# Optimization experiments

Measured on AMD Instinct MI355X. Metric: run time of the kernel, lower is better.

## Reference

```python
import jax, jax.numpy as jnp
import numpy as np

DIM = 384
HEADS = 12
WIN = (2, 7, 7)
MLP_RATIO = 4.0
EPS = 1e-5


def _rel_index(Wt, Wh, Ww):
    t, h, w = np.meshgrid(np.arange(Wt), np.arange(Wh), np.arange(Ww), indexing='ij')
    coords = np.stack([t, h, w]).reshape(3, -1).T  # (N,3)
    rel = coords[:, None] - coords[None]  # (N,N,3)
    rel[..., 0] += Wt - 1
    rel[..., 1] += Wh - 1
    rel[..., 2] += Ww - 1
    rel[..., 0] *= (2 * Wh - 1) * (2 * Ww - 1)
    rel[..., 1] *= (2 * Ww - 1)
    return rel.sum(-1)  # (N,N) int


def setup_inputs() -> dict:
    key = jax.random.key(0)
    ks = jax.random.split(key, 16)
    d = DIM
    hdim = int(d * MLP_RATIO)
    Wt, Wh, Ww = WIN
    table_size = (2 * Wt - 1) * (2 * Wh - 1) * (2 * Ww - 1)
    s = lambda fan: 1.0 / np.sqrt(fan)
    return {
        'x': jax.random.normal(ks[0], (2, 8, 56, 56, d), jnp.float32),
        'norm1_g': jnp.ones((d,), jnp.float32),
        'norm1_b': jnp.zeros((d,), jnp.float32),
        'qkv_w': jax.random.normal(ks[1], (d, 3 * d), jnp.float32) * s(d),
        'qkv_b': jnp.zeros((3 * d,), jnp.float32),
        'proj_w': jax.random.normal(ks[2], (d, d), jnp.float32) * s(d),
        'proj_b': jnp.zeros((d,), jnp.float32),
        'bias_table': jax.random.normal(ks[3], (table_size, HEADS), jnp.float32) * 0.02,
        'norm2_g': jnp.ones((d,), jnp.float32),
        'norm2_b': jnp.zeros((d,), jnp.float32),
        'fc1_w': jax.random.normal(ks[4], (d, hdim), jnp.float32) * s(d),
        'fc1_b': jnp.zeros((hdim,), jnp.float32),
        'fc2_w': jax.random.normal(ks[5], (hdim, d), jnp.float32) * s(hdim),
        'fc2_b': jnp.zeros((d,), jnp.float32),
        'rel_index': jnp.asarray(_rel_index(*WIN), jnp.int32),
    }


def _ln(x, g, b):
    mu = x.mean(-1, keepdims=True)
    var = ((x - mu) ** 2).mean(-1, keepdims=True)
    return (x - mu) * jax.lax.rsqrt(var + EPS) * g + b


def _window_partition(x, win):
    B, T, H, W, C = x.shape
    Wt, Wh, Ww = win
    x = x.reshape(B, T // Wt, Wt, H // Wh, Wh, W // Ww, Ww, C)
    x = x.transpose(0, 1, 3, 5, 2, 4, 6, 7)
    return x.reshape(-1, Wt * Wh * Ww, C)


def _window_reverse(win_x, win, B, T, H, W):
    Wt, Wh, Ww = win
    C = win_x.shape[-1]
    x = win_x.reshape(B, T // Wt, H // Wh, W // Ww, Wt, Wh, Ww, C)
    x = x.transpose(0, 1, 4, 2, 5, 3, 6, 7)
    return x.reshape(B, T, H, W, C)


def reference(x, norm1_g, norm1_b, qkv_w, qkv_b, proj_w, proj_b, bias_table,
              norm2_g, norm2_b, fc1_w, fc1_b, fc2_w, fc2_b, rel_index):
    B, T, H, W, C = x.shape
    Wt, Wh, Ww = WIN
    N = Wt * Wh * Ww
    shift = (Wt // 2, Wh // 2, Ww // 2)
    head_dim = C // HEADS
    scale = head_dim ** -0.5

    shortcut = x
    h = _ln(x, norm1_g, norm1_b)
    h = jnp.roll(h, shift=(-shift[0], -shift[1], -shift[2]), axis=(1, 2, 3))
    # dims chosen divisible by window -> no padding branch
    wins = _window_partition(h, WIN)  # (BnW, N, C)
    BnW = wins.shape[0]

    qkv = wins @ qkv_w + qkv_b  # (BnW, N, 3C)
    qkv = qkv.reshape(BnW, N, 3, HEADS, head_dim).transpose(2, 0, 3, 1, 4)
    q, k, v = qkv[0] * scale, qkv[1], qkv[2]  # (BnW, H, N, d)

    bias = bias_table[rel_index.reshape(-1)].reshape(N, N, HEADS).transpose(2, 0, 1)
    attn = jnp.einsum('bhnd,bhmd->bhnm', q, k) + bias[None]
    attn = jax.nn.softmax(attn, axis=-1)
    out = jnp.einsum('bhnm,bhmd->bhnd', attn, v)
    out = out.transpose(0, 2, 1, 3).reshape(BnW, N, C)
    out = out @ proj_w + proj_b

    h = _window_reverse(out.reshape(-1, Wt, Wh, Ww, C), WIN, B, T, H, W)
    h = jnp.roll(h, shift=shift, axis=(1, 2, 3))
    x = shortcut + h

    h2 = _ln(x, norm2_g, norm2_b)
    h2 = jax.nn.gelu(h2 @ fc1_w + fc1_b, approximate=False) @ fc2_w + fc2_b
    return x + h2
```

## Files before the change

### kernel.cpp

```cpp
#include <hip/hip_runtime.h>
#include <cstdint>
#include <cstddef>


typedef __bf16 bf16x8 __attribute__((ext_vector_type(8)));
typedef __bf16 bf16x4 __attribute__((ext_vector_type(4)));
typedef float f32x4 __attribute__((ext_vector_type(4)));

#define DIM 384
#define QKV_DIM 1152
#define HID 1536
#define NHEADS 12
#define NTOK 50176
#define NWIN 512

__device__ __forceinline__ void gload16(const void* g, void* s) {
  __builtin_amdgcn_global_load_lds(
      (const __attribute__((address_space(1))) void*)g,
      (__attribute__((address_space(3))) void*)s, 16, 0, 0);
}

__global__ __launch_bounds__(256) void build_tokmap_k(int* __restrict__ map) {
  int t = blockIdx.x * 256 + threadIdx.x;
  if (t >= NTOK) return;
  int win = t / 98, n = t - win * 98;
  int b = win >> 8, tw = (win >> 6) & 3, hw = (win >> 3) & 7, ww = win & 7;
  int dt = n / 49; int rem = n - dt * 49; int dh = rem / 7, dw = rem - dh * 7;
  int t0 = (tw * 2 + dt + 1) & 7;
  int h0 = hw * 7 + dh + 3; if (h0 >= 56) h0 -= 56;
  int w0 = ww * 7 + dw + 3; if (w0 >= 56) w0 -= 56;
  map[t] = ((b * 8 + t0) * 56 + h0) * 56 + w0;
}

__global__ __launch_bounds__(256) void expand_biasp_k(const float* __restrict__ table,
                                                      const int* __restrict__ rel,
                                                      float* __restrict__ out) {
  int e = blockIdx.x * 256 + threadIdx.x;
  if (e >= NHEADS * 49 * 256) return;
  int r = e & 3, l = (e >> 2) & 63;
  int rest = e >> 8;
  int ni = rest % 7, mi = (rest / 7) % 7, h = rest / 49;
  int i = mi * 16 + (l >> 4) * 4 + r;
  int j = ni * 16 + (l & 15);
  float v;
  if (j >= 98) v = -1e30f;
  else if (i >= 98) v = 0.f;
  else v = table[rel[i * 98 + j] * NHEADS + h];
  out[e] = v;
}

__global__ __launch_bounds__(256) void pack_w_k(const float* __restrict__ W,
                                                __bf16* __restrict__ WP,
                                                int K, int N, int nk,
                                                int scaleCols, float scale) {
  int idx = blockIdx.x * 256 + threadIdx.x;
  if (idx >= (K * N) >> 3) return;
  int l = idx & 63, f = (idx >> 6) & 7;
  int rest = idx >> 9, kt = rest % nk, cn = rest / nk;
  int n = f >> 1, kk = f & 1;
  int col = cn * 64 + n * 16 + (l & 15);
  int k0 = kt * 64 + (kk * 4 + (l >> 4)) * 8;
  float sc = (col < scaleCols) ? scale : 1.0f;
  bf16x8 v;
  #pragma unroll
  for (int j = 0; j < 8; ++j)
    v[j] = (__bf16)(W[(size_t)(k0 + j) * N + col] * sc);
  *(bf16x8*)(WP + (size_t)idx * 8) = v;
}

__global__ __launch_bounds__(256) void scale_bias_k(const float* __restrict__ b,
                                                    float* __restrict__ out,
                                                    int n, int scaleCols, float scale) {
  int e = blockIdx.x * 256 + threadIdx.x;
  if (e >= n) return;
  out[e] = b[e] * (e < scaleCols ? scale : 1.0f);
}

__global__ __launch_bounds__(384) void vtrans_k(const __bf16* __restrict__ qkv,
                                                __bf16* __restrict__ vt) {
  int win = blockIdx.x, t = threadIdx.x;
  const __bf16* base = qkv + (size_t)win * 98 * QKV_DIM + 768 + t;
  __bf16* orow = vt + ((size_t)win * 384 + t) * 128;
  #pragma unroll
  for (int c = 0; c < 16; ++c) {
    bf16x8 pk;
    #pragma unroll
    for (int e2 = 0; e2 < 8; ++e2) {
      int tok = c * 8 + e2;
      pk[e2] = (tok < 98) ? base[(size_t)tok * QKV_DIM] : (__bf16)0.f;
    }
    *(bf16x8*)(orow + c * 8) = pk;
  }
}

template <typename T>
__global__ __launch_bounds__(256) void ln_k(const T* __restrict__ x,
                                            const float* __restrict__ g,
                                            const float* __restrict__ bta,
                                            __bf16* __restrict__ out,
                                            const int* __restrict__ map) {
  int w = threadIdx.x >> 6, l = threadIdx.x & 63;
  int tok = blockIdx.x * 4 + w;
  int src = map ? map[tok] : tok;
  const T* row = x + (size_t)src * DIM;
  float v[6]; float s = 0.f;
  #pragma unroll
  for (int j = 0; j < 6; ++j) { v[j] = (float)row[l + 64 * j]; s += v[j]; }
  #pragma unroll
  for (int m = 1; m < 64; m <<= 1) s += __shfl_xor(s, m, 64);
  float mu = s * (1.f / DIM);
  float var = 0.f;
  #pragma unroll
  for (int j = 0; j < 6; ++j) { float d = v[j] - mu; var += d * d; }
  #pragma unroll
  for (int m = 1; m < 64; m <<= 1) var += __shfl_xor(var, m, 64);
  float rs = rsqrtf(var * (1.f / DIM) + 1e-5f);
  __bf16* orow = out + (size_t)tok * DIM;
  #pragma unroll
  for (int j = 0; j < 6; ++j) {
    int c = l + 64 * j;
    orow[c] = (__bf16)((v[j] - mu) * rs * g[c] + bta[c]);
  }
}

template <int EPI>
__global__ __launch_bounds__(256) void gemm_k(const __bf16* __restrict__ A,
                                              const __bf16* __restrict__ WP,
                                              const float* __restrict__ bias,
                                              int M, int N, int K,
                                              __bf16* __restrict__ outb,
                                              float* __restrict__ outf,
                                              const float* __restrict__ residf,
                                              const __bf16* __restrict__ residb,
                                              const int* __restrict__ tokmap) {
  __shared__ __align__(1024) char lds[32768];
  const int tid = threadIdx.x;
  const int l = tid & 63, w = tid >> 6;
  const int lr = l & 15, lg = l >> 4;
  const int ntile = N >> 6;
  const int nwg = gridDim.x, qd = nwg >> 3, rm = nwg & 7;
  const int xcd = blockIdx.x & 7;
  const int wgid = (xcd < rm ? xcd * (qd + 1) : rm * (qd + 1) + (xcd - rm) * qd)
                   + (blockIdx.x >> 3);
  const int bm = wgid / ntile, bn = wgid - bm * ntile;
  const int m0 = (bm << 8) + (w << 6);
  const int n0 = bn << 6;
  const int nk = K >> 6;
  const int sch = (l & 7) ^ ((l >> 3) & 7);
  const __bf16* pa = A + (size_t)(m0 + (l >> 3)) * K + sch * 8;
  char* abuf = lds + (w << 13);
  const __bf16* pB = WP + (size_t)bn * nk * 4096 + l * 8;

#define STAGEA(kt)                                                   \
  {                                                                  \
    const size_t ko_ = (size_t)(kt) << 6;                            \
    _Pragma("unroll")                                                \
    for (int s_ = 0; s_ < 8; ++s_)                                   \
      gload16(pa + (size_t)(s_ * 8) * K + ko_, abuf + s_ * 1024);    \
  }
#define LOADB(kt)                                                    \
  {                                                                  \
    const __bf16* p_ = pB + (size_t)(kt) * 4096;                     \
    _Pragma("unroll")                                                \
    for (int f_ = 0; f_ < 8; ++f_)                                   \
      b[f_] = *(const bf16x8*)(p_ + f_ * 512);                       \
  }
#define LDA()                                                        \
  {                                                                  \
    _Pragma("unroll")                                                \
    for (int kk_ = 0; kk_ < 2; ++kk_) {                              \
      const int ck_ = (kk_ << 2) + lg;                               \
      _Pragma("unroll")                                              \
      for (int m_ = 0; m_ < 4; ++m_) {                               \
        int r_ = (m_ << 4) + lr;                                     \
        a[m_][kk_] = *(const bf16x8*)(abuf + (r_ << 7) +             \
                                      ((ck_ ^ (r_ & 7)) << 4));      \
      }                                                              \
    }                                                                \
    asm volatile("s_waitcnt lgkmcnt(0)" ::: "memory");               \
    __builtin_amdgcn_sched_barrier(0);                               \
  }

  bf16x8 a[4][2], b[8];
  f32x4 acc[4][4] = {};

  STAGEA(0)
  asm volatile("s_waitcnt vmcnt(0)" ::: "memory");
  LDA()

  for (int kt = 0; kt < nk; ++kt) {
    LOADB(kt)
    const bool pf = (kt + 1 < nk);
    if (pf) STAGEA(kt + 1)
    __builtin_amdgcn_s_setprio(1);
    #pragma unroll
    for (int kk = 0; kk < 2; ++kk)
      #pragma unroll
      for (int m = 0; m < 4; ++m)
        #pragma unroll
        for (int n = 0; n < 4; ++n)
          acc[m][n] = __builtin_amdgcn_mfma_f32_16x16x32_bf16(b[n * 2 + kk], a[m][kk],
                                                              acc[m][n], 0, 0, 0);
    __builtin_amdgcn_s_setprio(0);
    if (pf) {
      asm volatile("s_waitcnt vmcnt(0)" ::: "memory");
      LDA()
    }
  }
#undef STAGEA
#undef LOADB
#undef LDA

  #pragma unroll
  for (int m = 0; m < 4; ++m) {
    const int grow = m0 + (m << 4) + lr;
    #pragma unroll
    for (int n = 0; n < 4; ++n) {
      const int gcol = n0 + (n << 4) + (lg << 2);
      f32x4 a4 = acc[m][n] + *(const f32x4*)(bias + gcol);
      if (EPI == 0) {
        bf16x4 c;
        #pragma unroll
        for (int r = 0; r < 4; ++r) c[r] = (__bf16)a4[r];
        *(bf16x4*)(outb + (size_t)grow * N + gcol) = c;
      } else if (EPI == 1) {
        int dst = tokmap[grow];
        f32x4 rv = *(const f32x4*)(residf + (size_t)dst * DIM + gcol);
        bf16x4 c;
        #pragma unroll
        for (int r = 0; r < 4; ++r) c[r] = (__bf16)(rv[r] + a4[r]);
        *(bf16x4*)(outb + (size_t)dst * DIM + gcol) = c;
      } else if (EPI == 2) {
        bf16x4 c;
        #pragma unroll
        for (int r = 0; r < 4; ++r) {
          float vv = a4[r];
          float y = vv * (1.0f + 0.044715f * vv * vv);
          c[r] = (__bf16)(vv / (1.0f + __expf(-1.5957691216057308f * y)));
        }
        *(bf16x4*)(outb + (size_t)grow * N + gcol) = c;
      } else {
        bf16x4 sv = *(const bf16x4*)(residb + (size_t)grow * N + gcol);
        f32x4 o;
        #pragma unroll
        for (int r = 0; r < 4; ++r) o[r] = (float)sv[r] + a4[r];
        *(f32x4*)(outf + (size_t)grow * N + gcol) = o;
      }
    }
  }
}

__global__ __launch_bounds__(64) void attn_k(const __bf16* __restrict__ qkv,
                                             const __bf16* __restrict__ vt,
                                             const float* __restrict__ pb,
                                             __bf16* __restrict__ out) {
  __shared__ __align__(1024) char P[4096];
  const int l = threadIdx.x, lr = l & 15, lg = l >> 4;
  const int bid = blockIdx.x;
  const int xc = bid & 7, kk = bid >> 3;
  const int wh = (kk / 7) * 8 + xc, mi = kk % 7;
  const int win = wh / NHEADS, h = wh - win * NHEADS;
  const size_t wbase = (size_t)win * 98 * QKV_DIM;
  const __bf16* qb = qkv + wbase + h * 32;
  const __bf16* kb = qb + 384;
  const bf16x8 z8 = {};
  const f32x4 fz = {};

  bf16x8 kf[7];
  #pragma unroll
  for (int ni = 0; ni < 7; ++ni) {
    int tok = ni * 16 + lr;
    kf[ni] = (tok < 98) ? *(const bf16x8*)(kb + (size_t)tok * QKV_DIM + lg * 8) : z8;
  }
  int qt = mi * 16 + lr;
  bf16x8 qf = (qt < 98) ? *(const bf16x8*)(qb + (size_t)qt * QKV_DIM + lg * 8) : z8;
  const f32x4* pbp = (const f32x4*)pb + (size_t)((h * 7 + mi) * 7) * 64 + l;
  f32x4 bv[7];
  #pragma unroll
  for (int ni = 0; ni < 7; ++ni) bv[ni] = pbp[ni * 64];

  f32x4 s[7];
  #pragma unroll
  for (int ni = 0; ni < 7; ++ni)
    s[ni] = __builtin_amdgcn_mfma_f32_16x16x32_bf16(qf, kf[ni], fz, 0, 0, 0);

  if (l < 32) {
    int row = l >> 1, c = 14 + (l & 1);
    *(f32x4*)(P + row * 256 + ((c ^ (row & 7)) << 4)) = fz;
  }

  #pragma unroll
  for (int r = 0; r < 4; ++r) {
    float mx = -1e30f;
    #pragma unroll
    for (int ni = 0; ni < 7; ++ni) {
      float vv = s[ni][r] + bv[ni][r];
      s[ni][r] = vv;
      mx = fmaxf(mx, vv);
    }
    #pragma unroll
    for (int m2 = 1; m2 < 16; m2 <<= 1) mx = fmaxf(mx, __shfl_xor(mx, m2, 64));
    float sum = 0.f;
    #pragma unroll
    for (int ni = 0; ni < 7; ++ni) { float p = __expf(s[ni][r] - mx); s[ni][r] = p; sum += p; }
    #pragma unroll
    for (int m2 = 1; m2 < 16; m2 <<= 1) sum += __shfl_xor(sum, m2, 64);
    float inv = 1.0f / sum;
    int il = lg * 4 + r;
    #pragma unroll
    for (int ni = 0; ni < 7; ++ni) {
      int j = ni * 16 + lr;
      *(__bf16*)(P + il * 256 + (((j >> 3) ^ (il & 7)) << 4) + ((j & 7) << 1)) =
          (__bf16)(s[ni][r] * inv);
    }
  }
  __syncthreads();

  bf16x8 pa[4];
  #pragma unroll
  for (int ks = 0; ks < 4; ++ks) {
    int ck = ks * 4 + lg;
    pa[ks] = *(const bf16x8*)(P + lr * 256 + ((ck ^ (lr & 7)) << 4));
  }
  const __bf16* vrow = vt + ((size_t)wh * 32) * 128;
  __bf16* ob = out + ((size_t)win * 98 + mi * 16) * DIM + h * 32;
  #pragma unroll
  for (int nf = 0; nf < 2; ++nf) {
    int d = nf * 16 + lr;
    f32x4 o = fz;
    #pragma unroll
    for (int ks = 0; ks < 4; ++ks) {
      bf16x8 vb = *(const bf16x8*)(vrow + (size_t)d * 128 + ks * 32 + lg * 8);
      o = __builtin_amdgcn_mfma_f32_16x16x32_bf16(pa[ks], vb, o, 0, 0, 0);
    }
    #pragma unroll
    for (int r = 0; r < 4; ++r) {
      int il = lg * 4 + r;
      if (mi * 16 + il < 98) ob[(size_t)il * DIM + nf * 16 + lr] = (__bf16)o[r];
    }
  }
}

extern "C" void kernel_launch(void* const* d_in, const int* in_sizes, int n_in,
                              void* d_out, int out_size, void* d_ws, size_t ws_size,
                              hipStream_t stream) {
  const float* x      = (const float*)d_in[0];
  const float* n1g    = (const float*)d_in[1];
  const float* n1b    = (const float*)d_in[2];
  const float* qkv_w  = (const float*)d_in[3];
  const float* qkv_b  = (const float*)d_in[4];
  const float* proj_w = (const float*)d_in[5];
  const float* proj_b = (const float*)d_in[6];
  const float* btab   = (const float*)d_in[7];
  const float* n2g    = (const float*)d_in[8];
  const float* n2b    = (const float*)d_in[9];
  const float* fc1_w  = (const float*)d_in[10];
  const float* fc1_b  = (const float*)d_in[11];
  const float* fc2_w  = (const float*)d_in[12];
  const float* fc2_b  = (const float*)d_in[13];
  const int*   relidx = (const int*)d_in[14];
  float* outp = (float*)d_out;
  (void)in_sizes; (void)n_in; (void)out_size; (void)ws_size;

  char* ws = (char*)d_ws;
  size_t off = 0;
  auto alloc = [&](size_t bytes) {
    char* p = ws + off;
    off = (off + bytes + 255) & ~(size_t)255;
    return p;
  };
  int*    tokmap = (int*)alloc((size_t)NTOK * 4);
  float*  biasex = (float*)alloc((size_t)NHEADS * 49 * 256 * 4);
  __bf16* wqkvP  = (__bf16*)alloc((size_t)QKV_DIM * DIM * 2);
  __bf16* wprojP = (__bf16*)alloc((size_t)DIM * DIM * 2);
  __bf16* wfc1P  = (__bf16*)alloc((size_t)HID * DIM * 2);
  __bf16* wfc2P  = (__bf16*)alloc((size_t)DIM * HID * 2);
  float*  qkvbS  = (float*)alloc((size_t)QKV_DIM * 4);
  __bf16* tokens = (__bf16*)alloc((size_t)NTOK * DIM * 2);
  __bf16* qkvbuf = (__bf16*)alloc((size_t)NTOK * HID * 2);
  __bf16* s1     = (__bf16*)alloc((size_t)NTOK * DIM * 2);
  __bf16* attnout = tokens;
  __bf16* h1 = qkvbuf;
  __bf16* vt = (__bf16*)d_out;

  const float scale = 0.17677669529663687f;

  build_tokmap_k<<<NTOK / 256, 256, 0, stream>>>(tokmap);
  expand_biasp_k<<<(NHEADS * 49 * 256) / 256, 256, 0, stream>>>(btab, relidx, biasex);
  pack_w_k<<<(DIM * QKV_DIM / 8) / 256, 256, 0, stream>>>(qkv_w, wqkvP, DIM, QKV_DIM, 6, DIM, scale);
  pack_w_k<<<(DIM * DIM / 8) / 256, 256, 0, stream>>>(proj_w, wprojP, DIM, DIM, 6, 0, 1.0f);
  pack_w_k<<<(DIM * HID / 8) / 256, 256, 0, stream>>>(fc1_w, wfc1P, DIM, HID, 6, 0, 1.0f);
  pack_w_k<<<(HID * DIM / 8) / 256, 256, 0, stream>>>(fc2_w, wfc2P, HID, DIM, 24, 0, 1.0f);
  scale_bias_k<<<(QKV_DIM + 255) / 256, 256, 0, stream>>>(qkv_b, qkvbS, QKV_DIM, DIM, scale);

  ln_k<float><<<NTOK / 4, 256, 0, stream>>>(x, n1g, n1b, tokens, tokmap);
  gemm_k<0><<<(NTOK / 256) * (QKV_DIM / 64), 256, 0, stream>>>(
      tokens, wqkvP, qkvbS, NTOK, QKV_DIM, DIM, qkvbuf, nullptr, nullptr, nullptr, nullptr);
  vtrans_k<<<NWIN, 384, 0, stream>>>(qkvbuf, vt);
  attn_k<<<NWIN * NHEADS * 7, 64, 0, stream>>>(qkvbuf, vt, biasex, attnout);
  gemm_k<1><<<(NTOK / 256) * (DIM / 64), 256, 0, stream>>>(
      attnout, wprojP, proj_b, NTOK, DIM, DIM, s1, nullptr, x, nullptr, tokmap);
  ln_k<__bf16><<<NTOK / 4, 256, 0, stream>>>(s1, n2g, n2b, tokens, nullptr);
  gemm_k<2><<<(NTOK / 256) * (HID / 64), 256, 0, stream>>>(
      tokens, wfc1P, fc1_b, NTOK, HID, DIM, h1, nullptr, nullptr, nullptr, nullptr);
  gemm_k<3><<<(NTOK / 256) * (DIM / 64), 256, 0, stream>>>(
      h1, wfc2P, fc2_b, NTOK, DIM, HID, nullptr, outp, nullptr, s1, nullptr);
}
```

Measured before the change: 520.7 us.

## Add A-stationary deep GEMM for K=384 layers and coalesce transposes via LDS

Adds a GEMM kernel for the K=384 layers (qkv, proj, fc1) in which each workgroup loads a 64-row A block once into LDS and loops over 128-column output groups. Weight fragments are double-buffered in registers, and the weights are repacked into a 128-wide layout to match. This removes the repeated A reloads of the old 256x64 tiling, at the cost of more LDS, more accumulators and less parallelism per workgroup. The V transpose and the attention output store now go through LDS, so global writes become full 16-byte rows instead of strided or scalar stores.

```diff
diff --git a/kernel.cpp b/kernel.cpp
--- a/kernel.cpp
+++ b/kernel.cpp
@@ -49,10 +49,28 @@
   out[e] = v;
 }
 
-__global__ __launch_bounds__(256) void pack_w_k(const float* __restrict__ W,
-                                                __bf16* __restrict__ WP,
-                                                int K, int N, int nk,
-                                                int scaleCols, float scale) {
+__global__ __launch_bounds__(256) void pack_w128_k(const float* __restrict__ W,
+                                                   __bf16* __restrict__ WP,
+                                                   int K, int N, int nk,
+                                                   int scaleCols, float scale) {
+  int idx = blockIdx.x * 256 + threadIdx.x;
+  if (idx >= (K * N) >> 3) return;
+  int l = idx & 63, f = (idx >> 6) & 7, wc = (idx >> 9) & 1;
+  int rest = idx >> 10, kt = rest % nk, bn = rest / nk;
+  int n = f >> 1, kk = f & 1;
+  int col = bn * 128 + wc * 64 + n * 16 + (l & 15);
+  int k0 = kt * 64 + (kk * 4 + (l >> 4)) * 8;
+  float sc = (col < scaleCols) ? scale : 1.0f;
+  bf16x8 v;
+  #pragma unroll
+  for (int j = 0; j < 8; ++j)
+    v[j] = (__bf16)(W[(size_t)(k0 + j) * N + col] * sc);
+  *(bf16x8*)(WP + (size_t)idx * 8) = v;
+}
+
+__global__ __launch_bounds__(256) void pack_w64_k(const float* __restrict__ W,
+                                                  __bf16* __restrict__ WP,
+                                                  int K, int N, int nk) {
   int idx = blockIdx.x * 256 + threadIdx.x;
   if (idx >= (K * N) >> 3) return;
   int l = idx & 63, f = (idx >> 6) & 7;
@@ -60,11 +78,10 @@
   int n = f >> 1, kk = f & 1;
   int col = cn * 64 + n * 16 + (l & 15);
   int k0 = kt * 64 + (kk * 4 + (l >> 4)) * 8;
-  float sc = (col < scaleCols) ? scale : 1.0f;
   bf16x8 v;
   #pragma unroll
   for (int j = 0; j < 8; ++j)
-    v[j] = (__bf16)(W[(size_t)(k0 + j) * N + col] * sc);
+    v[j] = (__bf16)W[(size_t)(k0 + j) * N + col];
   *(bf16x8*)(WP + (size_t)idx * 8) = v;
 }
 
@@ -78,9 +95,9 @@
 
 __global__ __launch_bounds__(384) void vtrans_k(const __bf16* __restrict__ qkv,
                                                 __bf16* __restrict__ vt) {
+  __shared__ __align__(1024) char T[98304];
   int win = blockIdx.x, t = threadIdx.x;
   const __bf16* base = qkv + (size_t)win * 98 * QKV_DIM + 768 + t;
-  __bf16* orow = vt + ((size_t)win * 384 + t) * 128;
   #pragma unroll
   for (int c = 0; c < 16; ++c) {
     bf16x8 pk;
@@ -89,7 +106,17 @@
       int tok = c * 8 + e2;
       pk[e2] = (tok < 98) ? base[(size_t)tok * QKV_DIM] : (__bf16)0.f;
     }
-    *(bf16x8*)(orow + c * 8) = pk;
+    *(bf16x8*)(T + t * 256 + ((c ^ (t & 15)) << 4)) = pk;
+  }
+  __syncthreads();
+  char* wb = (char*)(vt + (size_t)win * 49152);
+  #pragma unroll
+  for (int i = 0; i < 16; ++i) {
+    int g = i * 6144 + t * 16;
+    int row = g >> 8, p = (g >> 4) & 15;
+    bf16x8 v = *(const bf16x8*)(T + row * 256 + (p << 4));
+    int lc = p ^ (row & 15);
+    *(bf16x8*)(wb + row * 256 + (lc << 4)) = v;
   }
 }
 
@@ -124,16 +151,124 @@
 }
 
 template <int EPI>
-__global__ __launch_bounds__(256) void gemm_k(const __bf16* __restrict__ A,
-                                              const __bf16* __restrict__ WP,
-                                              const float* __restrict__ bias,
-                                              int M, int N, int K,
-                                              __bf16* __restrict__ outb,
-                                              float* __restrict__ outf,
-                                              const float* __restrict__ residf,
-                                              const __bf16* __restrict__ residb,
-                                              const int* __restrict__ tokmap) {
+__global__ __launch_bounds__(256) void gemm_deep_k(const __bf16* __restrict__ A,
+                                                   const __bf16* __restrict__ WP,
+                                                   const float* __restrict__ bias,
+                                                   int M, int N, int Gtot,
+                                                   __bf16* __restrict__ outb,
+                                                   const float* __restrict__ residf,
+                                                   const int* __restrict__ tokmap) {
+  __shared__ __align__(1024) char lds[49152];
+  const int K = 384;
+  const int tid = threadIdx.x;
+  const int l = tid & 63, w = tid >> 6;
+  const int lr = l & 15, lg = l >> 4;
+  const int bid = (blockIdx.x & 7) * (gridDim.x >> 3) + (blockIdx.x >> 3);
+  const int m0 = bid << 6;
+  const int sch = (l & 7) ^ ((l >> 3) & 7);
+  #pragma unroll
+  for (int i = 0; i < 12; ++i) {
+    const int c12 = w * 12 + i;
+    const int row = ((c12 & 7) << 3) + (l >> 3);
+    gload16(A + (size_t)(m0 + row) * K + ((c12 >> 3) << 6) + sch * 8,
+            lds + c12 * 1024);
+  }
+  __syncthreads();
+
+  const f32x4 fz4 = {};
+  f32x4 acc[4][8] = {};
+  bf16x8 b0[8], b1[8], af[4][2];
+
+#define LOADB(dst, p)                                          \
+  { _Pragma("unroll")                                          \
+    for (int f_ = 0; f_ < 8; ++f_)                             \
+      dst[f_] = *(const bf16x8*)((p) + f_ * 512); }
+#define LDA(kt)                                                \
+  { _Pragma("unroll")                                          \
+    for (int kk_ = 0; kk_ < 2; ++kk_) {                        \
+      const int ck_ = (kk_ << 2) + lg;                         \
+      _Pragma("unroll")                                        \
+      for (int m_ = 0; m_ < 4; ++m_) {                         \
+        const int r_ = (m_ << 4) + lr;                         \
+        af[m_][kk_] = *(const bf16x8*)(lds + (kt) * 8192 +     \
+            (r_ << 7) + ((ck_ ^ (r_ & 7)) << 4));              \
+      } }                                                      \
+    asm volatile("s_waitcnt lgkmcnt(0)" ::: "memory");         \
+    __builtin_amdgcn_sched_barrier(0); }
+#define MFMA_HALF(NOFF, B)                                     \
+  { __builtin_amdgcn_s_setprio(1);                             \
+    _Pragma("unroll")                                          \
+    for (int kk_ = 0; kk_ < 2; ++kk_)                          \
+      _Pragma("unroll")                                        \
+      for (int m_ = 0; m_ < 4; ++m_)                           \
+        _Pragma("unroll")                                      \
+        for (int n_ = 0; n_ < 4; ++n_)                         \
+          acc[m_][(NOFF) + n_] = __builtin_amdgcn_mfma_f32_16x16x32_bf16( \
+              B[n_ * 2 + kk_], af[m_][kk_], acc[m_][(NOFF) + n_], 0, 0, 0); \
+    __builtin_amdgcn_s_setprio(0); }
+
+  const __bf16* pg = WP + (size_t)w * 49152 + (size_t)l * 8;
+  if (w < Gtot) LOADB(b0, pg)
+  for (int g = w; g < Gtot; g += 4) {
+    #pragma unroll
+    for (int kt = 0; kt < 6; ++kt) {
+      const __bf16* ph = pg + kt * 8192;
+      LOADB(b1, ph + 4096)
+      LDA(kt)
+      MFMA_HALF(0, b0)
+      if (kt < 5) {
+        LOADB(b0, ph + 8192)
+      } else if (g + 4 < Gtot) {
+        LOADB(b0, pg + 4 * 49152)
+      }
+      MFMA_HALF(4, b1)
+    }
+    #pragma unroll
+    for (int m = 0; m < 4; ++m) {
+      const int grow = m0 + (m << 4) + lr;
+      #pragma unroll
+      for (int n = 0; n < 8; ++n) {
+        const int gcol = (g << 7) + (n << 4) + (lg << 2);
+        f32x4 a4 = acc[m][n] + *(const f32x4*)(bias + gcol);
+        acc[m][n] = fz4;
+        if (EPI == 0) {
+          bf16x4 c;
+          #pragma unroll
+          for (int r = 0; r < 4; ++r) c[r] = (__bf16)a4[r];
+          *(bf16x4*)(outb + (size_t)grow * N + gcol) = c;
+        } else if (EPI == 1) {
+          const int dst = tokmap[grow];
+          f32x4 rv = *(const f32x4*)(residf + (size_t)dst * DIM + gcol);
+          bf16x4 c;
+          #pragma unroll
+          for (int r = 0; r < 4; ++r) c[r] = (__bf16)(rv[r] + a4[r]);
+          *(bf16x4*)(outb + (size_t)dst * DIM + gcol) = c;
+        } else {
+          bf16x4 c;
+          #pragma unroll
+          for (int r = 0; r < 4; ++r) {
+            float vv = a4[r];
+            float y = vv * (1.0f + 0.044715f * vv * vv);
+            c[r] = (__bf16)(vv / (1.0f + __expf(-1.5957691216057308f * y)));
+          }
+          *(bf16x4*)(outb + (size_t)grow * N + gcol) = c;
+        }
+      }
+    }
+    pg += 4 * 49152;
+  }
+#undef LOADB
+#undef LDA
+#undef MFMA_HALF
+}
+
+__global__ __launch_bounds__(256) void gemm_fc2_k(const __bf16* __restrict__ A,
+                                                  const __bf16* __restrict__ WP,
+                                                  const float* __restrict__ bias,
+                                                  float* __restrict__ outf,
+                                                  const __bf16* __restrict__ residb) {
   __shared__ __align__(1024) char lds[32768];
+  const int M = NTOK, N = DIM, K = HID, nk = 24;
   const int tid = threadIdx.x;
   const int l = tid & 63, w = tid >> 6;
   const int lr = l & 15, lg = l >> 4;
@@ -145,29 +280,23 @@
   const int bm = wgid / ntile, bn = wgid - bm * ntile;
   const int m0 = (bm << 8) + (w << 6);
   const int n0 = bn << 6;
-  const int nk = K >> 6;
   const int sch = (l & 7) ^ ((l >> 3) & 7);
   const __bf16* pa = A + (size_t)(m0 + (l >> 3)) * K + sch * 8;
   char* abuf = lds + (w << 13);
   const __bf16* pB = WP + (size_t)bn * nk * 4096 + l * 8;
 
 #define STAGEA(kt)                                                   \
-  {                                                                  \
-    const size_t ko_ = (size_t)(kt) << 6;                            \
+  { const size_t ko_ = (size_t)(kt) << 6;                            \
     _Pragma("unroll")                                                \
     for (int s_ = 0; s_ < 8; ++s_)                                   \
-      gload16(pa + (size_t)(s_ * 8) * K + ko_, abuf + s_ * 1024);    \
-  }
+      gload16(pa + (size_t)(s_ * 8) * K + ko_, abuf + s_ * 1024); }
 #define LOADB(kt)                                                    \
-  {                                                                  \
-    const __bf16* p_ = pB + (size_t)(kt) * 4096;                     \
+  { const __bf16* p_ = pB + (size_t)(kt) * 4096;                     \
     _Pragma("unroll")                                                \
     for (int f_ = 0; f_ < 8; ++f_)                                   \
-      b[f_] = *(const bf16x8*)(p_ + f_ * 512);                       \
-  }
+      b[f_] = *(const bf16x8*)(p_ + f_ * 512); }
 #define LDA()                                                        \
-  {                                                                  \
-    _Pragma("unroll")                                                \
+  { _Pragma("unroll")                                                \
     for (int kk_ = 0; kk_ < 2; ++kk_) {                              \
       const int ck_ = (kk_ << 2) + lg;                               \
       _Pragma("unroll")                                              \
@@ -175,19 +304,15 @@
         int r_ = (m_ << 4) + lr;                                     \
         a[m_][kk_] = *(const bf16x8*)(abuf + (r_ << 7) +             \
                                       ((ck_ ^ (r_ & 7)) << 4));      \
-      }                                                              \
-    }                                                                \
+      } }                                                            \
     asm volatile("s_waitcnt lgkmcnt(0)" ::: "memory");               \
-    __builtin_amdgcn_sched_barrier(0);                               \
-  }
+    __builtin_amdgcn_sched_barrier(0); }
 
   bf16x8 a[4][2], b[8];
   f32x4 acc[4][4] = {};
-
   STAGEA(0)
   asm volatile("s_waitcnt vmcnt(0)" ::: "memory");
   LDA()
-
   for (int kt = 0; kt < nk; ++kt) {
     LOADB(kt)
     const bool pf = (kt + 1 < nk);
@@ -210,7 +335,6 @@
 #undef STAGEA
 #undef LOADB
 #undef LDA
-
   #pragma unroll
   for (int m = 0; m < 4; ++m) {
     const int grow = m0 + (m << 4) + lr;
@@ -218,34 +342,11 @@
     for (int n = 0; n < 4; ++n) {
       const int gcol = n0 + (n << 4) + (lg << 2);
       f32x4 a4 = acc[m][n] + *(const f32x4*)(bias + gcol);
-      if (EPI == 0) {
-        bf16x4 c;
-        #pragma unroll
-        for (int r = 0; r < 4; ++r) c[r] = (__bf16)a4[r];
-        *(bf16x4*)(outb + (size_t)grow * N + gcol) = c;
-      } else if (EPI == 1) {
-        int dst = tokmap[grow];
-        f32x4 rv = *(const f32x4*)(residf + (size_t)dst * DIM + gcol);
-        bf16x4 c;
-        #pragma unroll
-        for (int r = 0; r < 4; ++r) c[r] = (__bf16)(rv[r] + a4[r]);
-        *(bf16x4*)(outb + (size_t)dst * DIM + gcol) = c;
-      } else if (EPI == 2) {
-        bf16x4 c;
-        #pragma unroll
-        for (int r = 0; r < 4; ++r) {
-          float vv = a4[r];
-          float y = vv * (1.0f + 0.044715f * vv * vv);
-          c[r] = (__bf16)(vv / (1.0f + __expf(-1.5957691216057308f * y)));
-        }
-        *(bf16x4*)(outb + (size_t)grow * N + gcol) = c;
-      } else {
-        bf16x4 sv = *(const bf16x4*)(residb + (size_t)grow * N + gcol);
-        f32x4 o;
-        #pragma unroll
-        for (int r = 0; r < 4; ++r) o[r] = (float)sv[r] + a4[r];
-        *(f32x4*)(outf + (size_t)grow * N + gcol) = o;
-      }
+      bf16x4 sv = *(const bf16x4*)(residb + (size_t)grow * N + gcol);
+      f32x4 o;
+      #pragma unroll
+      for (int r = 0; r < 4; ++r) o[r] = (float)sv[r] + a4[r];
+      *(f32x4*)(outf + (size_t)grow * N + gcol) = o;
     }
   }
 }
@@ -323,7 +424,7 @@
     pa[ks] = *(const bf16x8*)(P + lr * 256 + ((ck ^ (lr & 7)) << 4));
   }
   const __bf16* vrow = vt + ((size_t)wh * 32) * 128;
-  __bf16* ob = out + ((size_t)win * 98 + mi * 16) * DIM + h * 32;
+  f32x4 oo[2];
   #pragma unroll
   for (int nf = 0; nf < 2; ++nf) {
     int d = nf * 16 + lr;
@@ -333,11 +434,21 @@
       bf16x8 vb = *(const bf16x8*)(vrow + (size_t)d * 128 + ks * 32 + lg * 8);
       o = __builtin_amdgcn_mfma_f32_16x16x32_bf16(pa[ks], vb, o, 0, 0, 0);
     }
-    #pragma unroll
-    for (int r = 0; r < 4; ++r) {
-      int il = lg * 4 + r;
-      if (mi * 16 + il < 98) ob[(size_t)il * DIM + nf * 16 + lr] = (__bf16)o[r];
-    }
+    oo[nf] = o;
+  }
+  #pragma unroll
+  for (int nf = 0; nf < 2; ++nf)
+    #pragma unroll
+    for (int r = 0; r < 4; ++r)
+      *(__bf16*)(P + (lg * 4 + r) * 64 + (((nf << 4) + lr) << 1)) = (__bf16)oo[nf][r];
+  asm volatile("s_waitcnt lgkmcnt(0)" ::: "memory");
+  __builtin_amdgcn_sched_barrier(0);
+  {
+    const int row = l >> 2;
+    bf16x8 v = *(const bf16x8*)(P + row * 64 + ((l & 3) << 4));
+    const int tok = mi * 16 + row;
+    if (tok < 98)
+      *(bf16x8*)(out + ((size_t)win * 98 + tok) * DIM + h * 32 + ((l & 3) << 3)) = v;
   }
 }
 
@@ -387,22 +498,22 @@
 
   build_tokmap_k<<<NTOK / 256, 256, 0, stream>>>(tokmap);
   expand_biasp_k<<<(NHEADS * 49 * 256) / 256, 256, 0, stream>>>(btab, relidx, biasex);
-  pack_w_k<<<(DIM * QKV_DIM / 8) / 256, 256, 0, stream>>>(qkv_w, wqkvP, DIM, QKV_DIM, 6, DIM, scale);
-  pack_w_k<<<(DIM * DIM / 8) / 256, 256, 0, stream>>>(proj_w, wprojP, DIM, DIM, 6, 0, 1.0f);
-  pack_w_k<<<(DIM * HID / 8) / 256, 256, 0, stream>>>(fc1_w, wfc1P, DIM, HID, 6, 0, 1.0f);
-  pack_w_k<<<(HID * DIM / 8) / 256, 256, 0, stream>>>(fc2_w, wfc2P, HID, DIM, 24, 0, 1.0f);
+  pack_w128_k<<<(DIM * QKV_DIM / 8) / 256, 256, 0, stream>>>(qkv_w, wqkvP, DIM, QKV_DIM, 6, DIM, scale);
+  pack_w128_k<<<(DIM * DIM / 8) / 256, 256, 0, stream>>>(proj_w, wprojP, DIM, DIM, 6, 0, 1.0f);
+  pack_w128_k<<<(DIM * HID / 8) / 256, 256, 0, stream>>>(fc1_w, wfc1P, DIM, HID, 6, 0, 1.0f);
+  pack_w64_k<<<(HID * DIM / 8) / 256, 256, 0, stream>>>(fc2_w, wfc2P, HID, DIM, 24);
   scale_bias_k<<<(QKV_DIM + 255) / 256, 256, 0, stream>>>(qkv_b, qkvbS, QKV_DIM, DIM, scale);
 
   ln_k<float><<<NTOK / 4, 256, 0, stream>>>(x, n1g, n1b, tokens, tokmap);
-  gemm_k<0><<<(NTOK / 256) * (QKV_DIM / 64), 256, 0, stream>>>(
-      tokens, wqkvP, qkvbS, NTOK, QKV_DIM, DIM, qkvbuf, nullptr, nullptr, nullptr, nullptr);
+  gemm_deep_k<0><<<NTOK / 64, 256, 0, stream>>>(
+      tokens, wqkvP, qkvbS, NTOK, QKV_DIM, QKV_DIM / 128, qkvbuf, nullptr, nullptr);
   vtrans_k<<<NWIN, 384, 0, stream>>>(qkvbuf, vt);
   attn_k<<<NWIN * NHEADS * 7, 64, 0, stream>>>(qkvbuf, vt, biasex, attnout);
-  gemm_k<1><<<(NTOK / 256) * (DIM / 64), 256, 0, stream>>>(
-      attnout, wprojP, proj_b, NTOK, DIM, DIM, s1, nullptr, x, nullptr, tokmap);
+  gemm_deep_k<1><<<NTOK / 64, 256, 0, stream>>>(
+      attnout, wprojP, proj_b, NTOK, DIM, DIM / 128, s1, x, tokmap);
   ln_k<__bf16><<<NTOK / 4, 256, 0, stream>>>(s1, n2g, n2b, tokens, nullptr);
-  gemm_k<2><<<(NTOK / 256) * (HID / 64), 256, 0, stream>>>(
-      tokens, wfc1P, fc1_b, NTOK, HID, DIM, h1, nullptr, nullptr, nullptr, nullptr);
-  gemm_k<3><<<(NTOK / 256) * (DIM / 64), 256, 0, stream>>>(
-      h1, wfc2P, fc2_b, NTOK, DIM, HID, nullptr, outp, nullptr, s1, nullptr);
-}
+  gemm_deep_k<2><<<NTOK / 64, 256, 0, stream>>>(
+      tokens, wfc1P, fc1_b, NTOK, HID, HID / 128, h1, nullptr, nullptr);
+  gemm_fc2_k<<<(NTOK / 256) * (DIM / 64), 256, 0, stream>>>(
+      h1, wfc2P, fc2_b, outp, s1);
+}
```

New measurement: 595.5 us. 14.3% more time.
